# Performance work log

Measured on AMD Instinct MI355X. Metric: run time of the kernel, lower is better.

## Reference

```python
import jax, jax.numpy as jnp
import numpy as np

B, S, HID = 4, 2048, 512
NH, HD = 8, 64          # num heads, head dim (num_kv_heads == NH, so GQA group = 1)
SW = 250                # sliding window
THETA = 10000.0
SCALING = 1.0 / np.sqrt(HD)
NEG_INF = jnp.finfo(jnp.float32).min


def setup_inputs() -> dict:
    key = jax.random.key(0)
    ks = jax.random.split(key, 5)
    w_std = 1.0 / np.sqrt(HID)
    return {
        "hidden_states": jax.random.normal(ks[0], (B, S, HID), jnp.float32),
        "position_ids": jnp.broadcast_to(jnp.arange(S, dtype=jnp.int64), (B, S)),
        "Wq": jax.random.normal(ks[1], (NH * HD, HID), jnp.float32) * w_std,
        "Wk": jax.random.normal(ks[2], (NH * HD, HID), jnp.float32) * w_std,
        "Wv": jax.random.normal(ks[3], (NH * HD, HID), jnp.float32) * w_std,
        "Wo": jax.random.normal(ks[4], (HID, NH * HD), jnp.float32) * w_std,
    }


def _rotate_half(x):
    x1, x2 = jnp.split(x, 2, axis=-1)
    return jnp.concatenate((-x2, x1), axis=-1)


def reference(hidden_states, position_ids, Wq, Wk, Wv, Wo):
    b, s, _ = hidden_states.shape
    dtype = hidden_states.dtype

    # QKV projections (Linear: x @ W.T, no bias) -> [b, h, s, d]
    q = (hidden_states @ Wq.T).reshape(b, s, NH, HD).transpose(0, 2, 1, 3)
    k = (hidden_states @ Wk.T).reshape(b, s, NH, HD).transpose(0, 2, 1, 3)
    v = (hidden_states @ Wv.T).reshape(b, s, NH, HD).transpose(0, 2, 1, 3)

    # Rotary embedding (MimiRotaryEmbedding), computed in fp32
    inv_freq = 1.0 / (THETA ** (jnp.arange(0, HD, 2, dtype=jnp.float32) / HD))
    freqs = position_ids.astype(jnp.float32)[:, :, None] * inv_freq[None, None, :]  # [b, s, HD/2]
    emb = jnp.concatenate((freqs, freqs), axis=-1)                                   # [b, s, HD]
    cos = jnp.cos(emb).astype(dtype)[:, None, :, :]  # unsqueeze head dim
    sin = jnp.sin(emb).astype(dtype)[:, None, :, :]
    q = q * cos + _rotate_half(q) * sin
    k = k * cos + _rotate_half(k) * sin

    # Sliding-window causal additive mask: keep kv iff q_idx >= kv_idx and q_idx - kv_idx <= SW
    idx = jnp.arange(s)
    keep = (idx[:, None] >= idx[None, :]) & ((idx[:, None] - idx[None, :]) <= SW)
    bias = jnp.where(keep, 0.0, NEG_INF).astype(jnp.float32)  # [s, s]

    # Eager attention: full scores, fp32 softmax (num_key_value_groups == 1)
    scores = jnp.einsum("bhqd,bhkd->bhqk", q, k) * SCALING
    scores = scores.astype(jnp.float32) + bias[None, None, :, :]
    attn = jax.nn.softmax(scores, axis=-1).astype(dtype)
    out = jnp.einsum("bhqk,bhkd->bhqd", attn, v)

    # merge heads and output projection
    out = out.transpose(0, 2, 1, 3).reshape(b, s, NH * HD)
    return out @ Wo.T
```

## Files before the change

kernel.cpp:

```cpp
#include <hip/hip_runtime.h>
#include <hip/hip_bf16.h>
#include <math.h>


#define B_   4
#define S_   2048
#define HID_ 512
#define NH_  8
#define HD_  64
#define SW_  250

typedef __bf16 bf16x8 __attribute__((ext_vector_type(8)));
typedef __bf16 bf16x4 __attribute__((ext_vector_type(4)));
typedef float f32x4 __attribute__((ext_vector_type(4)));
using bf16_t = __hip_bfloat16;
typedef unsigned int u32;

__device__ __forceinline__ void glds16(const void* g, void* l) {
    __builtin_amdgcn_global_load_lds(
        (const __attribute__((address_space(1))) u32*)g,
        (__attribute__((address_space(3))) u32*)l, 16, 0, 0);
}

__global__ __launch_bounds__(256) void cvt_all(
    const float* __restrict__ X,  const float* __restrict__ Wq,
    const float* __restrict__ Wk, const float* __restrict__ Wv,
    const float* __restrict__ Wo,
    bf16_t* __restrict__ Xb, bf16_t* __restrict__ Wcat, bf16_t* __restrict__ Wob)
{
    const int blk = blockIdx.x;
    const float* s; bf16_t* d; size_t base;
    if (blk < 2048)      { s = X;  d = Xb;            base = (size_t)blk * 2048; }
    else if (blk < 2176) { s = Wq; d = Wcat;          base = (size_t)(blk - 2048) * 2048; }
    else if (blk < 2304) { s = Wk; d = Wcat + 262144; base = (size_t)(blk - 2176) * 2048; }
    else if (blk < 2432) { s = Wv; d = Wcat + 524288; base = (size_t)(blk - 2304) * 2048; }
    else                 { s = Wo; d = Wob;           base = (size_t)(blk - 2432) * 2048; }
    size_t i = base + (size_t)threadIdx.x * 8;
    float4 a = *reinterpret_cast<const float4*>(s + i);
    float4 b = *reinterpret_cast<const float4*>(s + i + 4);
    bf16x8 r;
    r[0] = (__bf16)a.x; r[1] = (__bf16)a.y; r[2] = (__bf16)a.z; r[3] = (__bf16)a.w;
    r[4] = (__bf16)b.x; r[5] = (__bf16)b.y; r[6] = (__bf16)b.z; r[7] = (__bf16)b.w;
    *reinterpret_cast<bf16x8*>(d + i) = r;
}

__global__ __launch_bounds__(256) void qkv_gemm(
    const bf16_t* __restrict__ Xb, const bf16_t* __restrict__ Wcat,
    bf16_t* __restrict__ Q, bf16_t* __restrict__ Kbuf, bf16_t* __restrict__ Vt)
{
    __shared__ __align__(16) char smem_raw[34816];
    bf16_t* As = (bf16_t*)smem_raw;
    bf16_t* Bs = As + 4096;
    const int tid = threadIdx.x;
    const int wave = tid >> 6, lane = tid & 63;
    const int quad = lane >> 4, l16 = lane & 15;
    const int wm = wave & 1, wn = wave >> 1;
    const int m0 = blockIdx.x * 128, n0 = blockIdx.y * 128;

    f32x4 acc[4][4] = {};
    for (int k0 = 0; k0 < HID_; k0 += 32) {
#pragma unroll
        for (int rr = 0; rr < 2; ++rr) {
            int slot = rr * 256 + tid;
            int row = slot >> 2;
            int l = (slot & 3) ^ ((row >> 1) & 3);
            glds16(Xb + (size_t)(m0 + row) * HID_ + k0 + l * 8, As + slot * 8);
            glds16(Wcat + (size_t)(n0 + row) * HID_ + k0 + l * 8, Bs + slot * 8);
        }
        __syncthreads();
        bf16x8 af[4], bfr[4];
#pragma unroll
        for (int i = 0; i < 4; ++i) {
            int ra = wm * 64 + i * 16 + l16;
            int rb = wn * 64 + i * 16 + l16;
            int pa = quad ^ ((ra >> 1) & 3);
            int pb = quad ^ ((rb >> 1) & 3);
            af[i]  = *reinterpret_cast<const bf16x8*>(&As[ra * 32 + pa * 8]);
            bfr[i] = *reinterpret_cast<const bf16x8*>(&Bs[rb * 32 + pb * 8]);
        }
#pragma unroll
        for (int mi = 0; mi < 4; ++mi)
#pragma unroll
            for (int ni = 0; ni < 4; ++ni)
                acc[mi][ni] = __builtin_amdgcn_mfma_f32_16x16x32_bf16(af[mi], bfr[ni], acc[mi][ni], 0, 0, 0);
        __syncthreads();
    }

    const int seg = n0 >> 9;
    const int hh = ((n0 & 511) + wn * 64) >> 6;
    bf16_t* wt = (bf16_t*)smem_raw + wave * 4352;
    const int mbase = m0 + wm * 64;
    const int bb = mbase >> 11;
    const int sbase = mbase & (S_ - 1);

    if (seg < 2) {
        const float qs = (seg == 0) ? 0.125f : 1.0f;
        const float c = 0.41524101186f;
        float inv0 = exp2f(-(float)l16 * c);
        float inv1 = exp2f(-(float)(l16 + 16) * c);
#pragma unroll
        for (int mi = 0; mi < 4; ++mi)
#pragma unroll
            for (int r = 0; r < 4; ++r) {
                int lrow = mi * 16 + quad * 4 + r;
                float sf = (float)(sbase + lrow);
#pragma unroll
                for (int ip = 0; ip < 2; ++ip) {
                    float sn, cs_;
                    __sincosf(sf * (ip ? inv1 : inv0), &sn, &cs_);
                    float x1 = acc[mi][ip][r], x2 = acc[mi][ip + 2][r];
                    wt[lrow * 68 + ip * 16 + l16]      = __float2bfloat16((x1 * cs_ - x2 * sn) * qs);
                    wt[lrow * 68 + ip * 16 + l16 + 32] = __float2bfloat16((x2 * cs_ + x1 * sn) * qs);
                }
            }
        bf16_t* Y = (seg == 0) ? Q : Kbuf;
#pragma unroll
        for (int it = 0; it < 8; ++it) {
            int e = it * 64 + lane;
            int sr = e >> 3, doff = (e & 7) * 8;
            size_t g = ((size_t)(bb * NH_ + hh) * S_ + sbase + sr) * HD_ + doff;
            *reinterpret_cast<bf16x8*>(Y + g) =
                *reinterpret_cast<const bf16x8*>(wt + sr * 68 + doff);
        }
    } else {
#pragma unroll
        for (int mi = 0; mi < 4; ++mi)
#pragma unroll
            for (int ni = 0; ni < 4; ++ni)
#pragma unroll
                for (int r = 0; r < 4; ++r)
                    wt[(ni * 16 + l16) * 68 + mi * 16 + quad * 4 + r] =
                        __float2bfloat16(acc[mi][ni][r]);
#pragma unroll
        for (int it = 0; it < 8; ++it) {
            int e = it * 64 + lane;
            int d = e >> 3, soff = (e & 7) * 8;
            size_t g = ((size_t)(bb * NH_ + hh) * HD_ + d) * S_ + sbase + soff;
            *reinterpret_cast<bf16x8*>(Vt + g) =
                *reinterpret_cast<const bf16x8*>(wt + d * 68 + soff);
        }
    }
}

__global__ __launch_bounds__(256) void attn_mfma(
    const bf16_t* __restrict__ Q, const bf16_t* __restrict__ K,
    const bf16_t* __restrict__ Vt, bf16_t* __restrict__ A)
{
    __shared__ __align__(16) __bf16 pt[4][16][296];
    __shared__ float sums_l[4][16];
    const int wave = threadIdx.x >> 6, lane = threadIdx.x & 63;
    const int quad = lane >> 4, l16 = lane & 15;
    const int h = blockIdx.y, b = blockIdx.z;
    const int q0 = (blockIdx.x * 4 + wave) * 16;
    const size_t bh  = (size_t)(b * NH_ + h) * S_;
    const size_t bhd = (size_t)(b * NH_ + h) * HD_;

    bf16x8 qf0, qf1;
    {
        const bf16_t* qp = Q + (bh + q0 + l16) * HD_ + quad * 8;
        qf0 = *reinterpret_cast<const bf16x8*>(qp);
        qf1 = *reinterpret_cast<const bf16x8*>(qp + 32);
    }
    const int kstart = (q0 > SW_) ? ((q0 - SW_) & ~31) : 0;
    const int nt = (q0 + 15 - kstart + 32) >> 5;
    const int qq = q0 + l16;

    f32x4 s[9][2];
#pragma unroll
    for (int t = 0; t < 9; ++t) {
        if (t < nt) {
            const int kb = kstart + t * 32;
#pragma unroll
            for (int half = 0; half < 2; ++half) {
                const bf16_t* kp = K + (bh + kb + half * 16 + l16) * HD_ + quad * 8;
                bf16x8 k0 = *reinterpret_cast<const bf16x8*>(kp);
                bf16x8 k1 = *reinterpret_cast<const bf16x8*>(kp + 32);
                f32x4 z = {};
                z = __builtin_amdgcn_mfma_f32_16x16x32_bf16(k0, qf0, z, 0, 0, 0);
                z = __builtin_amdgcn_mfma_f32_16x16x32_bf16(k1, qf1, z, 0, 0, 0);
                const int kbase = kb + half * 16 + quad * 4;
#pragma unroll
                for (int r = 0; r < 4; ++r) {
                    int key = kbase + r;
                    bool keep = (key <= qq) && (qq - key <= SW_);
                    s[t][half][r] = keep ? z[r] : -3.0e38f;
                }
            }
        }
    }
    float mx = -3.0e38f;
#pragma unroll
    for (int t = 0; t < 9; ++t)
        if (t < nt)
#pragma unroll
            for (int half = 0; half < 2; ++half)
#pragma unroll
                for (int r = 0; r < 4; ++r)
                    mx = fmaxf(mx, s[t][half][r]);
    mx = fmaxf(mx, __shfl_xor(mx, 16, 64));
    mx = fmaxf(mx, __shfl_xor(mx, 32, 64));

    float sum = 0.f;
#pragma unroll
    for (int t = 0; t < 9; ++t)
        if (t < nt)
#pragma unroll
            for (int half = 0; half < 2; ++half) {
                bf16x4 pk;
#pragma unroll
                for (int r = 0; r < 4; ++r) {
                    float p = __expf(s[t][half][r] - mx);
                    sum += p;
                    pk[r] = (__bf16)p;
                }
                *reinterpret_cast<bf16x4*>(&pt[wave][l16][t * 32 + half * 16 + quad * 4]) = pk;
            }
    sum += __shfl_xor(sum, 16, 64);
    sum += __shfl_xor(sum, 32, 64);
    if (quad == 0) sums_l[wave][l16] = sum;

    f32x4 o[4] = {};
#pragma unroll
    for (int t = 0; t < 9; ++t) {
        if (t < nt) {
            const int kb = kstart + t * 32;
            bf16x8 pf = *reinterpret_cast<const bf16x8*>(&pt[wave][l16][t * 32 + quad * 8]);
#pragma unroll
            for (int nf = 0; nf < 4; ++nf) {
                const bf16_t* vp = Vt + (bhd + nf * 16 + l16) * S_ + kb + quad * 8;
                bf16x8 vf = *reinterpret_cast<const bf16x8*>(vp);
                o[nf] = __builtin_amdgcn_mfma_f32_16x16x32_bf16(pf, vf, o[nf], 0, 0, 0);
            }
        }
    }
    float inv_l[4];
#pragma unroll
    for (int r = 0; r < 4; ++r) inv_l[r] = 1.0f / sums_l[wave][quad * 4 + r];
#pragma unroll
    for (int nf = 0; nf < 4; ++nf)
#pragma unroll
        for (int r = 0; r < 4; ++r) {
            int qr = q0 + quad * 4 + r;
            A[((size_t)(b * S_ + qr)) * HID_ + h * HD_ + nf * 16 + l16] =
                __float2bfloat16(o[nf][r] * inv_l[r]);
        }
}

__global__ __launch_bounds__(256) void out_proj(
    const bf16_t* __restrict__ Ain, const bf16_t* __restrict__ Wob,
    float* __restrict__ out)
{
    __shared__ __align__(16) bf16_t As[128 * 32];
    __shared__ __align__(16) bf16_t Bs[64 * 32];
    const int tid = threadIdx.x;
    const int wave = tid >> 6, lane = tid & 63;
    const int quad = lane >> 4, l16 = lane & 15;
    const int m0 = blockIdx.x * 128, n0 = blockIdx.y * 64;

    f32x4 acc[2][4] = {};
    for (int k0 = 0; k0 < HID_; k0 += 32) {
#pragma unroll
        for (int rr = 0; rr < 2; ++rr) {
            int slot = rr * 256 + tid;
            int row = slot >> 2;
            int l = (slot & 3) ^ ((row >> 1) & 3);
            glds16(Ain + (size_t)(m0 + row) * HID_ + k0 + l * 8, As + slot * 8);
        }
        {
            int slot = tid;
            int row = slot >> 2;
            int l = (slot & 3) ^ ((row >> 1) & 3);
            glds16(Wob + (size_t)(n0 + row) * HID_ + k0 + l * 8, Bs + slot * 8);
        }
        __syncthreads();
        bf16x8 af[2], bfr[4];
#pragma unroll
        for (int i = 0; i < 2; ++i) {
            int ra = wave * 32 + i * 16 + l16;
            int pa = quad ^ ((ra >> 1) & 3);
            af[i] = *reinterpret_cast<const bf16x8*>(&As[ra * 32 + pa * 8]);
        }
#pragma unroll
        for (int i = 0; i < 4; ++i) {
            int rb = i * 16 + l16;
            int pb = quad ^ ((rb >> 1) & 3);
            bfr[i] = *reinterpret_cast<const bf16x8*>(&Bs[rb * 32 + pb * 8]);
        }
#pragma unroll
        for (int mi = 0; mi < 2; ++mi)
#pragma unroll
            for (int ni = 0; ni < 4; ++ni)
                acc[mi][ni] = __builtin_amdgcn_mfma_f32_16x16x32_bf16(af[mi], bfr[ni], acc[mi][ni], 0, 0, 0);
        __syncthreads();
    }
#pragma unroll
    for (int mi = 0; mi < 2; ++mi)
#pragma unroll
        for (int ni = 0; ni < 4; ++ni)
#pragma unroll
            for (int r = 0; r < 4; ++r) {
                int m = m0 + wave * 32 + mi * 16 + quad * 4 + r;
                int n = n0 + ni * 16 + l16;
                out[(size_t)m * HID_ + n] = acc[mi][ni][r];
            }
}

extern "C" void kernel_launch(void* const* d_in, const int* in_sizes, int n_in,
                              void* d_out, int out_size, void* d_ws, size_t ws_size,
                              hipStream_t stream)
{
    const float* X  = (const float*)d_in[0];
    const float* Wq = (const float*)d_in[2];
    const float* Wk = (const float*)d_in[3];
    const float* Wv = (const float*)d_in[4];
    const float* Wo = (const float*)d_in[5];

    char* ws = (char*)d_ws;
    const size_t elems = (size_t)B_ * NH_ * S_ * HD_;
    const size_t wsz   = (size_t)HID_ * HID_;
    bf16_t* Q    = (bf16_t*)ws;
    bf16_t* K    = Q + elems;
    bf16_t* Vt   = K + elems;
    bf16_t* Xb   = Vt + elems;
    bf16_t* A    = Xb;
    bf16_t* Wcat = Xb + elems;
    bf16_t* Wob  = Wcat + 3 * wsz;

    cvt_all<<<2560, 256, 0, stream>>>(X, Wq, Wk, Wv, Wo, Xb, Wcat, Wob);
    qkv_gemm<<<dim3(64, 12), 256, 0, stream>>>(Xb, Wcat, Q, K, Vt);
    attn_mfma<<<dim3(32, 8, 4), 256, 0, stream>>>(Q, K, Vt, A);
    out_proj<<<dim3(64, 8), 256, 0, stream>>>(A, Wob, (float*)d_out);
}
```

Before: 144.3 us.

## Double GEMM K-step to 64 and stage epilogue stores through LDS

The QKV and output-projection GEMMs now load 64-wide K slices per barrier pair, using a new 8-way XOR swizzle, which halves the number of sync iterations. The attention and out_proj epilogues write their results to per-wave LDS tiles first and then issue 16-byte row-contiguous global stores in place of scattered 2- and 4-byte writes. This trades more LDS per block, which could lower occupancy, and an extra LDS round trip for better coalescing and fewer barriers.

```diff
diff --git a/kernel.cpp b/kernel.cpp
--- a/kernel.cpp
+++ b/kernel.cpp
@@ -50,7 +50,7 @@
 {
     __shared__ __align__(16) char smem_raw[34816];
     bf16_t* As = (bf16_t*)smem_raw;
-    bf16_t* Bs = As + 4096;
+    bf16_t* Bs = As + 8192;
     const int tid = threadIdx.x;
     const int wave = tid >> 6, lane = tid & 63;
     const int quad = lane >> 4, l16 = lane & 15;
@@ -58,31 +58,35 @@
     const int m0 = blockIdx.x * 128, n0 = blockIdx.y * 128;
 
     f32x4 acc[4][4] = {};
-    for (int k0 = 0; k0 < HID_; k0 += 32) {
-#pragma unroll
-        for (int rr = 0; rr < 2; ++rr) {
+    for (int k0 = 0; k0 < HID_; k0 += 64) {
+#pragma unroll
+        for (int rr = 0; rr < 4; ++rr) {
             int slot = rr * 256 + tid;
-            int row = slot >> 2;
-            int l = (slot & 3) ^ ((row >> 1) & 3);
+            int row = slot >> 3;
+            int l = (slot & 7) ^ (row & 7);
             glds16(Xb + (size_t)(m0 + row) * HID_ + k0 + l * 8, As + slot * 8);
             glds16(Wcat + (size_t)(n0 + row) * HID_ + k0 + l * 8, Bs + slot * 8);
         }
         __syncthreads();
-        bf16x8 af[4], bfr[4];
-#pragma unroll
-        for (int i = 0; i < 4; ++i) {
-            int ra = wm * 64 + i * 16 + l16;
-            int rb = wn * 64 + i * 16 + l16;
-            int pa = quad ^ ((ra >> 1) & 3);
-            int pb = quad ^ ((rb >> 1) & 3);
-            af[i]  = *reinterpret_cast<const bf16x8*>(&As[ra * 32 + pa * 8]);
-            bfr[i] = *reinterpret_cast<const bf16x8*>(&Bs[rb * 32 + pb * 8]);
-        }
-#pragma unroll
-        for (int mi = 0; mi < 4; ++mi)
-#pragma unroll
-            for (int ni = 0; ni < 4; ++ni)
-                acc[mi][ni] = __builtin_amdgcn_mfma_f32_16x16x32_bf16(af[mi], bfr[ni], acc[mi][ni], 0, 0, 0);
+#pragma unroll
+        for (int kk = 0; kk < 2; ++kk) {
+            bf16x8 af[4], bfr[4];
+#pragma unroll
+            for (int i = 0; i < 4; ++i) {
+                int ra = wm * 64 + i * 16 + l16;
+                int rb = wn * 64 + i * 16 + l16;
+                int c = kk * 4 + quad;
+                int pa = c ^ (ra & 7);
+                int pb = c ^ (rb & 7);
+                af[i]  = *reinterpret_cast<const bf16x8*>(&As[ra * 64 + pa * 8]);
+                bfr[i] = *reinterpret_cast<const bf16x8*>(&Bs[rb * 64 + pb * 8]);
+            }
+#pragma unroll
+            for (int mi = 0; mi < 4; ++mi)
+#pragma unroll
+                for (int ni = 0; ni < 4; ++ni)
+                    acc[mi][ni] = __builtin_amdgcn_mfma_f32_16x16x32_bf16(af[mi], bfr[ni], acc[mi][ni], 0, 0, 0);
+        }
         __syncthreads();
     }
 
@@ -236,73 +240,93 @@
     float inv_l[4];
 #pragma unroll
     for (int r = 0; r < 4; ++r) inv_l[r] = 1.0f / sums_l[wave][quad * 4 + r];
+
+    __bf16* at = &pt[wave][0][0];
 #pragma unroll
     for (int nf = 0; nf < 4; ++nf)
 #pragma unroll
-        for (int r = 0; r < 4; ++r) {
-            int qr = q0 + quad * 4 + r;
-            A[((size_t)(b * S_ + qr)) * HID_ + h * HD_ + nf * 16 + l16] =
+        for (int r = 0; r < 4; ++r)
+            at[(quad * 4 + r) * 72 + nf * 16 + l16] =
                 __float2bfloat16(o[nf][r] * inv_l[r]);
-        }
+#pragma unroll
+    for (int it = 0; it < 2; ++it) {
+        int e = it * 64 + lane;
+        int sr = e >> 3, doff = (e & 7) * 8;
+        *reinterpret_cast<bf16x8*>(
+            A + ((size_t)(b * S_) + q0 + sr) * HID_ + h * HD_ + doff) =
+            *reinterpret_cast<const bf16x8*>(at + sr * 72 + doff);
+    }
 }
 
 __global__ __launch_bounds__(256) void out_proj(
     const bf16_t* __restrict__ Ain, const bf16_t* __restrict__ Wob,
     float* __restrict__ out)
 {
-    __shared__ __align__(16) bf16_t As[128 * 32];
-    __shared__ __align__(16) bf16_t Bs[64 * 32];
+    __shared__ __align__(16) char smem_raw[34816];
+    bf16_t* As = (bf16_t*)smem_raw;
+    bf16_t* Bs = As + 8192;
     const int tid = threadIdx.x;
     const int wave = tid >> 6, lane = tid & 63;
     const int quad = lane >> 4, l16 = lane & 15;
     const int m0 = blockIdx.x * 128, n0 = blockIdx.y * 64;
 
     f32x4 acc[2][4] = {};
-    for (int k0 = 0; k0 < HID_; k0 += 32) {
+    for (int k0 = 0; k0 < HID_; k0 += 64) {
+#pragma unroll
+        for (int rr = 0; rr < 4; ++rr) {
+            int slot = rr * 256 + tid;
+            int row = slot >> 3;
+            int l = (slot & 7) ^ (row & 7);
+            glds16(Ain + (size_t)(m0 + row) * HID_ + k0 + l * 8, As + slot * 8);
+        }
 #pragma unroll
         for (int rr = 0; rr < 2; ++rr) {
             int slot = rr * 256 + tid;
-            int row = slot >> 2;
-            int l = (slot & 3) ^ ((row >> 1) & 3);
-            glds16(Ain + (size_t)(m0 + row) * HID_ + k0 + l * 8, As + slot * 8);
-        }
-        {
-            int slot = tid;
-            int row = slot >> 2;
-            int l = (slot & 3) ^ ((row >> 1) & 3);
+            int row = slot >> 3;
+            int l = (slot & 7) ^ (row & 7);
             glds16(Wob + (size_t)(n0 + row) * HID_ + k0 + l * 8, Bs + slot * 8);
         }
         __syncthreads();
-        bf16x8 af[2], bfr[4];
-#pragma unroll
-        for (int i = 0; i < 2; ++i) {
-            int ra = wave * 32 + i * 16 + l16;
-            int pa = quad ^ ((ra >> 1) & 3);
-            af[i] = *reinterpret_cast<const bf16x8*>(&As[ra * 32 + pa * 8]);
-        }
-#pragma unroll
-        for (int i = 0; i < 4; ++i) {
-            int rb = i * 16 + l16;
-            int pb = quad ^ ((rb >> 1) & 3);
-            bfr[i] = *reinterpret_cast<const bf16x8*>(&Bs[rb * 32 + pb * 8]);
-        }
-#pragma unroll
-        for (int mi = 0; mi < 2; ++mi)
-#pragma unroll
-            for (int ni = 0; ni < 4; ++ni)
-                acc[mi][ni] = __builtin_amdgcn_mfma_f32_16x16x32_bf16(af[mi], bfr[ni], acc[mi][ni], 0, 0, 0);
+#pragma unroll
+        for (int kk = 0; kk < 2; ++kk) {
+            bf16x8 af[2], bfr[4];
+#pragma unroll
+            for (int i = 0; i < 2; ++i) {
+                int ra = wave * 32 + i * 16 + l16;
+                int pa = (kk * 4 + quad) ^ (ra & 7);
+                af[i] = *reinterpret_cast<const bf16x8*>(&As[ra * 64 + pa * 8]);
+            }
+#pragma unroll
+            for (int i = 0; i < 4; ++i) {
+                int rb = i * 16 + l16;
+                int pb = (kk * 4 + quad) ^ (rb & 7);
+                bfr[i] = *reinterpret_cast<const bf16x8*>(&Bs[rb * 64 + pb * 8]);
+            }
+#pragma unroll
+            for (int mi = 0; mi < 2; ++mi)
+#pragma unroll
+                for (int ni = 0; ni < 4; ++ni)
+                    acc[mi][ni] = __builtin_amdgcn_mfma_f32_16x16x32_bf16(af[mi], bfr[ni], acc[mi][ni], 0, 0, 0);
+        }
         __syncthreads();
     }
+
+    float* ot = (float*)smem_raw + wave * 2176;
 #pragma unroll
     for (int mi = 0; mi < 2; ++mi)
 #pragma unroll
         for (int ni = 0; ni < 4; ++ni)
 #pragma unroll
-            for (int r = 0; r < 4; ++r) {
-                int m = m0 + wave * 32 + mi * 16 + quad * 4 + r;
-                int n = n0 + ni * 16 + l16;
-                out[(size_t)m * HID_ + n] = acc[mi][ni][r];
-            }
+            for (int r = 0; r < 4; ++r)
+                ot[(mi * 16 + quad * 4 + r) * 68 + ni * 16 + l16] = acc[mi][ni][r];
+#pragma unroll
+    for (int it = 0; it < 8; ++it) {
+        int e = it * 64 + lane;
+        int sr = e >> 4, f4 = (e & 15) * 4;
+        int m = m0 + wave * 32 + sr;
+        *reinterpret_cast<float4*>(&out[(size_t)m * HID_ + n0 + f4]) =
+            *reinterpret_cast<const float4*>(&ot[sr * 68 + f4]);
+    }
 }
 
 extern "C" void kernel_launch(void* const* d_in, const int* in_sizes, int n_in,
```

Result: slower. 149.5 us (+3.6%).

## Split each query tile's key range across waves with LDS softmax merge

Applied to the files above, without the earlier changes.

Each attention block now owns a single 16-query tile, and its four waves take interleaved 32-key tiles instead of each wave covering every key tile for its own queries. Each wave keeps a partial max, sum and output, writes them to shared memory, and the block merges them with a rescaled log-sum-exp combine before writing A. This cuts per-wave score registers from 18 to 6 vectors and launches four times as many blocks, aiming for higher occupancy and better latency hiding. The cost is an extra block-wide sync, more shared memory for the partial outputs, and repeated Q loads across waves.

```diff
diff --git a/kernel.cpp b/kernel.cpp
--- a/kernel.cpp
+++ b/kernel.cpp
@@ -146,12 +146,14 @@
     const bf16_t* __restrict__ Q, const bf16_t* __restrict__ K,
     const bf16_t* __restrict__ Vt, bf16_t* __restrict__ A)
 {
-    __shared__ __align__(16) __bf16 pt[4][16][296];
-    __shared__ float sums_l[4][16];
+    __shared__ __align__(16) __bf16 pt[4][16][104];
+    __shared__ __align__(16) float O_ws[4][16][66];
+    __shared__ float m_l[4][16];
+    __shared__ float s_l[4][16];
     const int wave = threadIdx.x >> 6, lane = threadIdx.x & 63;
     const int quad = lane >> 4, l16 = lane & 15;
     const int h = blockIdx.y, b = blockIdx.z;
-    const int q0 = (blockIdx.x * 4 + wave) * 16;
+    const int q0 = blockIdx.x * 16;
     const size_t bh  = (size_t)(b * NH_ + h) * S_;
     const size_t bhd = (size_t)(b * NH_ + h) * HD_;
 
@@ -163,13 +165,14 @@
     }
     const int kstart = (q0 > SW_) ? ((q0 - SW_) & ~31) : 0;
     const int nt = (q0 + 15 - kstart + 32) >> 5;
+    const int ntl = (nt > wave) ? ((nt - wave + 3) >> 2) : 0;
     const int qq = q0 + l16;
 
-    f32x4 s[9][2];
-#pragma unroll
-    for (int t = 0; t < 9; ++t) {
-        if (t < nt) {
-            const int kb = kstart + t * 32;
+    f32x4 s[3][2];
+#pragma unroll
+    for (int j = 0; j < 3; ++j) {
+        if (j < ntl) {
+            const int kb = kstart + (wave + 4 * j) * 32;
 #pragma unroll
             for (int half = 0; half < 2; ++half) {
                 const bf16_t* kp = K + (bh + kb + half * 16 + l16) * HD_ + quad * 8;
@@ -183,48 +186,48 @@
                 for (int r = 0; r < 4; ++r) {
                     int key = kbase + r;
                     bool keep = (key <= qq) && (qq - key <= SW_);
-                    s[t][half][r] = keep ? z[r] : -3.0e38f;
+                    s[j][half][r] = keep ? z[r] : -3.0e38f;
                 }
             }
         }
     }
     float mx = -3.0e38f;
 #pragma unroll
-    for (int t = 0; t < 9; ++t)
-        if (t < nt)
+    for (int j = 0; j < 3; ++j)
+        if (j < ntl)
 #pragma unroll
             for (int half = 0; half < 2; ++half)
 #pragma unroll
                 for (int r = 0; r < 4; ++r)
-                    mx = fmaxf(mx, s[t][half][r]);
+                    mx = fmaxf(mx, s[j][half][r]);
     mx = fmaxf(mx, __shfl_xor(mx, 16, 64));
     mx = fmaxf(mx, __shfl_xor(mx, 32, 64));
 
     float sum = 0.f;
 #pragma unroll
-    for (int t = 0; t < 9; ++t)
-        if (t < nt)
+    for (int j = 0; j < 3; ++j)
+        if (j < ntl)
 #pragma unroll
             for (int half = 0; half < 2; ++half) {
                 bf16x4 pk;
 #pragma unroll
                 for (int r = 0; r < 4; ++r) {
-                    float p = __expf(s[t][half][r] - mx);
+                    float p = __expf(s[j][half][r] - mx);
                     sum += p;
                     pk[r] = (__bf16)p;
                 }
-                *reinterpret_cast<bf16x4*>(&pt[wave][l16][t * 32 + half * 16 + quad * 4]) = pk;
+                *reinterpret_cast<bf16x4*>(&pt[wave][l16][j * 32 + half * 16 + quad * 4]) = pk;
             }
     sum += __shfl_xor(sum, 16, 64);
     sum += __shfl_xor(sum, 32, 64);
-    if (quad == 0) sums_l[wave][l16] = sum;
+    if (quad == 0) { m_l[wave][l16] = mx; s_l[wave][l16] = sum; }
 
     f32x4 o[4] = {};
 #pragma unroll
-    for (int t = 0; t < 9; ++t) {
-        if (t < nt) {
-            const int kb = kstart + t * 32;
-            bf16x8 pf = *reinterpret_cast<const bf16x8*>(&pt[wave][l16][t * 32 + quad * 8]);
+    for (int j = 0; j < 3; ++j) {
+        if (j < ntl) {
+            const int kb = kstart + (wave + 4 * j) * 32;
+            bf16x8 pf = *reinterpret_cast<const bf16x8*>(&pt[wave][l16][j * 32 + quad * 8]);
 #pragma unroll
             for (int nf = 0; nf < 4; ++nf) {
                 const bf16_t* vp = Vt + (bhd + nf * 16 + l16) * S_ + kb + quad * 8;
@@ -233,17 +236,27 @@
             }
         }
     }
-    float inv_l[4];
-#pragma unroll
-    for (int r = 0; r < 4; ++r) inv_l[r] = 1.0f / sums_l[wave][quad * 4 + r];
 #pragma unroll
     for (int nf = 0; nf < 4; ++nf)
 #pragma unroll
-        for (int r = 0; r < 4; ++r) {
-            int qr = q0 + quad * 4 + r;
-            A[((size_t)(b * S_ + qr)) * HID_ + h * HD_ + nf * 16 + l16] =
-                __float2bfloat16(o[nf][r] * inv_l[r]);
-        }
+        for (int r = 0; r < 4; ++r)
+            O_ws[wave][quad * 4 + r][nf * 16 + l16] = o[nf][r];
+    __syncthreads();
+
+    const int d = wave * 16 + l16;
+#pragma unroll
+    for (int r = 0; r < 4; ++r) {
+        const int q = quad * 4 + r;
+        float m0v = m_l[0][q], m1v = m_l[1][q], m2v = m_l[2][q], m3v = m_l[3][q];
+        float M = fmaxf(fmaxf(m0v, m1v), fmaxf(m2v, m3v));
+        float e0 = __expf(m0v - M), e1 = __expf(m1v - M);
+        float e2 = __expf(m2v - M), e3 = __expf(m3v - M);
+        float lt = s_l[0][q] * e0 + s_l[1][q] * e1 + s_l[2][q] * e2 + s_l[3][q] * e3;
+        float ov = O_ws[0][q][d] * e0 + O_ws[1][q][d] * e1
+                 + O_ws[2][q][d] * e2 + O_ws[3][q][d] * e3;
+        A[((size_t)(b * S_ + q0 + q)) * HID_ + h * HD_ + d] =
+            __float2bfloat16(ov / lt);
+    }
 }
 
 __global__ __launch_bounds__(256) void out_proj(
@@ -328,6 +341,6 @@
 
     cvt_all<<<2560, 256, 0, stream>>>(X, Wq, Wk, Wv, Wo, Xb, Wcat, Wob);
     qkv_gemm<<<dim3(64, 12), 256, 0, stream>>>(Xb, Wcat, Q, K, Vt);
-    attn_mfma<<<dim3(32, 8, 4), 256, 0, stream>>>(Q, K, Vt, A);
+    attn_mfma<<<dim3(128, 8, 4), 256, 0, stream>>>(Q, K, Vt, A);
     out_proj<<<dim3(64, 8), 256, 0, stream>>>(A, Wob, (float*)d_out);
 }
```

New measurement: 149.6 us. 1.04x slower.
